# Optimization experiments

Measured on AMD Instinct MI355X. Metric: run time of the kernel, lower is better.

Reference implementation:

```python
import jax, jax.numpy as jnp
import numpy as np

B, M, K = 8192, 1024, 2048
R_LR = 0.1
LMDA = 1e-12
TOL = 0.01          # relative-change convergence threshold from the torch code
MAX_ITERS = 10000   # safety cap (torch loop is uncapped; see notes)


def setup_inputs() -> dict:
    key = jax.random.key(0)
    k_img, k_w = jax.random.split(key)
    img_batch = jax.random.normal(k_img, (B, M), dtype=jnp.float32)
    # U.weight is [M, K]; normalize_weights() normalizes columns (dim=0)
    W = jax.random.normal(k_w, (M, K), dtype=jnp.float32)
    W = W / jnp.linalg.norm(W, axis=0, keepdims=True)
    return {"img_batch": img_batch, "W": W}


def _soft_threshold(x, lmda):
    # F.relu(x - l) - F.relu(-x - l): shrink magnitudes toward zero by l
    return jax.nn.relu(x - lmda) - jax.nn.relu(-x - lmda)


def _inference(img_batch, W):
    Bn, Mn = img_batch.shape
    Kn = W.shape[1]
    # MSELoss(reduction='mean'): dL/dpred = 2*(pred - img)/(B*M)
    scale = 2.0 / (Bn * Mn)

    def cond_fun(state):
        _, it, done = state
        # torch: `while not converged`; nan (first iter, ||old_r||=0) -> not done
        return jnp.logical_and(jnp.logical_not(done), it < MAX_ITERS)

    def body_fun(state):
        r, it, _ = state  # r plays the role of old_r for this step
        pred = r @ W.T                       # [B, M], U(r)
        grad_r = scale * ((pred - img_batch) @ W)  # [B, K], analytic MSE grad
        r_new = _soft_threshold(r - R_LR * grad_r, LMDA)
        ratio = jnp.linalg.norm(r_new - r) / jnp.linalg.norm(r)
        return (r_new, it + 1, ratio < TOL)

    r0 = jnp.zeros((Bn, Kn), dtype=img_batch.dtype)
    r, _, _ = jax.lax.while_loop(
        cond_fun, body_fun, (r0, jnp.array(0, jnp.int32), jnp.array(False)))
    return r


def reference(img_batch, W):
    r = _inference(img_batch, W)   # ISTA loop (no grad flows out, as in torch)
    pred = r @ W.T                 # final decode U(r)
    return (r, pred)
```

## Files before the change

### kernel.cpp

```cpp
#include <hip/hip_runtime.h>

#define NB 8192
#define NM 1024
#define NK 2048

typedef unsigned short ushort_t;
using bf16x8 = __attribute__((ext_vector_type(8))) short;
using f32x4  = __attribute__((ext_vector_type(4))) float;

__device__ __forceinline__ float alpha_const() {
  const double s = 0.1 * (2.0 / 8388608.0);
  return (float)(101.0 * s);
}

__device__ __forceinline__ ushort_t f2bf(float f) {
  union { float f; unsigned u; } v; v.f = f;
  unsigned r = (v.u + 0x7FFFu + ((v.u >> 16) & 1u)) >> 16;
  return (ushort_t)r;
}

__device__ __forceinline__ void gload_lds16(const void* g, void* l) {
  __builtin_amdgcn_global_load_lds(
      (const __attribute__((address_space(1))) unsigned int*)g,
      (__attribute__((address_space(3))) unsigned int*)l, 16, 0, 0);
}

__global__ __launch_bounds__(256)
void prep_w_k(const float* __restrict__ W, ushort_t* __restrict__ Wbf,
              ushort_t* __restrict__ Wt)
{
  __shared__ ushort_t tile[64][65];
  const int tid = threadIdx.x;
  const int bW = blockIdx.x;
  const int m0 = (bW >> 5) * 64, k0 = (bW & 31) * 64;
  const int r = tid >> 2, q = tid & 3;
  ushort_t loc[16];
#pragma unroll
  for (int j = 0; j < 4; ++j) {
    const float4 v = *(const float4*)&W[(size_t)(m0 + r) * NK + k0 + q * 16 + j * 4];
    loc[j * 4 + 0] = f2bf(v.x); loc[j * 4 + 1] = f2bf(v.y);
    loc[j * 4 + 2] = f2bf(v.z); loc[j * 4 + 3] = f2bf(v.w);
  }
#pragma unroll
  for (int j = 0; j < 4; ++j) {
    ushort4 o;
    o.x = loc[j * 4 + 0]; o.y = loc[j * 4 + 1];
    o.z = loc[j * 4 + 2]; o.w = loc[j * 4 + 3];
    *(ushort4*)&Wbf[(size_t)(m0 + r) * NK + k0 + q * 16 + j * 4] = o;
  }
#pragma unroll
  for (int jj = 0; jj < 16; ++jj) tile[r][q * 16 + jj] = loc[jj];
  __syncthreads();
  const int kk = tid >> 2, qq = tid & 3;
#pragma unroll
  for (int j = 0; j < 4; ++j) {
    ushort4 o;
    o.x = tile[qq * 16 + j * 4 + 0][kk];
    o.y = tile[qq * 16 + j * 4 + 1][kk];
    o.z = tile[qq * 16 + j * 4 + 2][kk];
    o.w = tile[qq * 16 + j * 4 + 3][kk];
    *(ushort4*)&Wt[(size_t)(k0 + kk) * NM + m0 + qq * 16 + j * 4] = o;
  }
}

__global__ __launch_bounds__(256)
void qimg_k(const ushort_t* __restrict__ Wbf, ushort_t* __restrict__ Qbf,
            const float* __restrict__ img, ushort_t* __restrict__ imgbf)
{
  __shared__ __align__(128) ushort_t As[64 * 64];
  __shared__ __align__(128) ushort_t Bs[64 * 64];
  const int tid = threadIdx.x;
  const int b = blockIdx.x;

  if (b >= 256) {
    const int base = (b - 256) * 2048;
#pragma unroll
    for (int i = 0; i < 8; ++i) {
      const int idx = base + i * 256 + tid;
      const float4 v = ((const float4*)img)[idx];
      ushort4 o;
      o.x = f2bf(v.x); o.y = f2bf(v.y); o.z = f2bf(v.z); o.w = f2bf(v.w);
      ((ushort4*)imgbf)[idx] = o;
    }
    return;
  }

  const int w = tid >> 6, l = tid & 63;
  const int wm2 = w >> 1, wn2 = w & 1;
  const int bi = b >> 4, bj = b & 15;
  const int i0 = bi * 64, j0 = bj * 64;
  const int l15 = l & 15, l16 = l >> 4;
  const int lr = l >> 3;
  const int lc = (l & 7) * 8;

  f32x4 acc[2][2];
#pragma unroll
  for (int m = 0; m < 2; ++m)
#pragma unroll
    for (int n = 0; n < 2; ++n)
      acc[m][n] = (f32x4){0.f, 0.f, 0.f, 0.f};

  for (int k0 = 0; k0 < NK; k0 += 64) {
#pragma unroll
    for (int c = 0; c < 2; ++c) {
      const int rr = c * 32 + w * 8 + lr;
      const int base = c * 2048 + w * 512;
      gload_lds16(Wbf + (size_t)(i0 + rr) * NK + k0 + lc, &As[base]);
      gload_lds16(Wbf + (size_t)(j0 + rr) * NK + k0 + lc, &Bs[base]);
    }
    __syncthreads();
#pragma unroll
    for (int ks = 0; ks < 2; ++ks) {
      bf16x8 af[2], bfr[2];
#pragma unroll
      for (int m = 0; m < 2; ++m)
        af[m] = *(const bf16x8*)&As[(wm2 * 32 + m * 16 + l15) * 64 + ks * 32 + l16 * 8];
#pragma unroll
      for (int n = 0; n < 2; ++n)
        bfr[n] = *(const bf16x8*)&Bs[(wn2 * 32 + n * 16 + l15) * 64 + ks * 32 + l16 * 8];
#pragma unroll
      for (int m = 0; m < 2; ++m)
#pragma unroll
        for (int n = 0; n < 2; ++n)
          acc[m][n] = __builtin_amdgcn_mfma_f32_16x16x32_bf16(af[m], bfr[n], acc[m][n], 0, 0, 0);
    }
    __syncthreads();
  }

#pragma unroll
  for (int m = 0; m < 2; ++m)
#pragma unroll
    for (int n = 0; n < 2; ++n) {
      const int gr0 = i0 + wm2 * 32 + m * 16 + l16 * 4;
      const int gc  = j0 + wn2 * 32 + n * 16 + l15;
#pragma unroll
      for (int q = 0; q < 4; ++q)
        Qbf[(size_t)(gr0 + q) * NM + gc] = f2bf(acc[m][n][q]);
    }
}

template<int BN>
__device__ __forceinline__
void gemm8ph_body(char* smem,
                  const ushort_t* __restrict__ Aop, const ushort_t* __restrict__ Bop,
                  int KK, int njb, int outld, float* __restrict__ outf,
                  int bid, int nblk)
{
  constexpr int WN  = BN / 4;
  constexpr int NFR = BN / 64;

  const int tid = threadIdx.x;
  const int w = tid >> 6, l = tid & 63;
  const int wm = w >> 2, wn = w & 3;
  const int wg = (bid & 7) * (nblk >> 3) + (bid >> 3);
  const int bi = wg / njb, bj = wg % njb;
  const int i0 = bi * 256, j0 = bj * BN;
  const int l15 = l & 15, l16 = l >> 4;
  const int srow8 = l >> 3;
  const int scb   = (l & 7) << 4;

  const float al = alpha_const();

  ushort_t* ldsA = (ushort_t*)smem;
  ushort_t* ldsB = (ushort_t*)(smem + 65536);
  constexpr int ASTR = 256 * 64;
  constexpr int BSTR = BN * 64;

  f32x4 acc[8][NFR];
#pragma unroll
  for (int m = 0; m < 8; ++m)
#pragma unroll
    for (int n = 0; n < NFR; ++n)
      acc[m][n] = (f32x4){0.f, 0.f, 0.f, 0.f};
  bf16x8 Bf[NFR][2];

  auto SH2 = [&](ushort_t* lb, const ushort_t* g0) {
#pragma unroll
    for (int c = 0; c < 2; ++c) {
      const int row = (w * 2 + c) * 8 + srow8;
      const int sc = (scb ^ ((row & 7) << 4)) >> 1;
      gload_lds16(g0 + (size_t)row * (size_t)KK + sc, lb + (w * 2 + c) * 512);
    }
  };
  auto SH1 = [&](ushort_t* lb, const ushort_t* g0) {
    const int row = w * 8 + srow8;
    const int sc = (scb ^ ((row & 7) << 4)) >> 1;
    gload_lds16(g0 + (size_t)row * (size_t)KK + sc, lb + w * 512);
  };
  auto stA = [&](int buf, int half, int kt) {
    SH2(ldsA + buf * ASTR + half * (128 * 64),
        Aop + (size_t)(i0 + half * 128) * (size_t)KK + (size_t)kt * 64);
  };
  auto stB = [&](int buf, int half, int kt) {
    if constexpr (BN == 256)
      SH2(ldsB + buf * BSTR + half * (128 * 64),
          Bop + (size_t)(j0 + half * 128) * (size_t)KK + (size_t)kt * 64);
    else
      SH1(ldsB + buf * BSTR + half * (64 * 64),
          Bop + (size_t)(j0 + half * 64) * (size_t)KK + (size_t)kt * 64);
  };
  auto rdA = [&](int buf, int R, int ks) -> bf16x8 {
    const int bc = ((ks * 64 + l16 * 16) ^ ((R & 7) << 4)) >> 1;
    return *(const bf16x8*)&ldsA[buf * ASTR + R * 64 + bc];
  };
  auto rdB = [&](int buf, int R, int ks) -> bf16x8 {
    const int bc = ((ks * 64 + l16 * 16) ^ ((R & 7) << 4)) >> 1;
    return *(const bf16x8*)&ldsB[buf * BSTR + R * 64 + bc];
  };

#define VMC_STEADY() do { \
    if constexpr (BN == 256) asm volatile("s_waitcnt vmcnt(4)" ::: "memory"); \
    else                     asm volatile("s_waitcnt vmcnt(2)" ::: "memory"); } while (0)

#define STOREQ(qd)                                                          \
  do {                                                                      \
    _Pragma("unroll")                                                       \
    for (int mm = 0; mm < 2; ++mm) {                                        \
      const int m = (qd) * 2 + mm;                                          \
      const int gr0 = i0 + wm * 128 + m * 16 + l16 * 4;                     \
      _Pragma("unroll")                                                     \
      for (int n = 0; n < NFR; ++n) {                                       \
        const int gc = j0 + wn * WN + n * 16 + l15;                         \
        _Pragma("unroll")                                                   \
        for (int qq = 0; qq < 4; ++qq) {                                    \
          const size_t idx = (size_t)(gr0 + qq) * (size_t)outld + gc;       \
          outf[idx] = al * acc[m][n][qq];                                   \
        }                                                                   \
      }                                                                     \
    }                                                                       \
  } while (0)

#define PHASE(bufc, q, LB, STG, VM, EPI)                                    \
  do {                                                                      \
    if (LB) {                                                               \
      _Pragma("unroll")                                                     \
      for (int n = 0; n < NFR; ++n) {                                       \
        Bf[n][0] = rdB(bufc, wn * WN + n * 16 + l15, 0);                    \
        Bf[n][1] = rdB(bufc, wn * WN + n * 16 + l15, 1);                    \
      }                                                                     \
    }                                                                       \
    bf16x8 a00 = rdA(bufc, wm * 128 + ((q) * 2 + 0) * 16 + l15, 0);         \
    bf16x8 a01 = rdA(bufc, wm * 128 + ((q) * 2 + 0) * 16 + l15, 1);         \
    bf16x8 a10 = rdA(bufc, wm * 128 + ((q) * 2 + 1) * 16 + l15, 0);         \
    bf16x8 a11 = rdA(bufc, wm * 128 + ((q) * 2 + 1) * 16 + l15, 1);         \
    STG;                                                                    \
    if (LB && BN == 256) asm volatile("s_waitcnt lgkmcnt(8)" ::: "memory"); \
    __builtin_amdgcn_s_barrier();                                           \
    asm volatile("s_waitcnt lgkmcnt(0)" ::: "memory");                      \
    __builtin_amdgcn_sched_barrier(0);                                      \
    __builtin_amdgcn_s_setprio(1);                                          \
    _Pragma("unroll")                                                       \
    for (int n = 0; n < NFR; ++n) {                                         \
      acc[(q) * 2 + 0][n] = __builtin_amdgcn_mfma_f32_16x16x32_bf16(        \
          a00, Bf[n][0], acc[(q) * 2 + 0][n], 0, 0, 0);                     \
      acc[(q) * 2 + 0][n] = __builtin_amdgcn_mfma_f32_16x16x32_bf16(        \
          a01, Bf[n][1], acc[(q) * 2 + 0][n], 0, 0, 0);                     \
      acc[(q) * 2 + 1][n] = __builtin_amdgcn_mfma_f32_16x16x32_bf16(        \
          a10, Bf[n][0], acc[(q) * 2 + 1][n], 0, 0, 0);                     \
      acc[(q) * 2 + 1][n] = __builtin_amdgcn_mfma_f32_16x16x32_bf16(        \
          a11, Bf[n][1], acc[(q) * 2 + 1][n], 0, 0, 0);                     \
    }                                                                       \
    __builtin_amdgcn_s_setprio(0);                                          \
    EPI;                                                                    \
    {                                                                       \
      const int _vm = (VM);                                                 \
      if (_vm == 1) VMC_STEADY();                                           \
      else if (_vm == 2) asm volatile("s_waitcnt vmcnt(0)" ::: "memory");   \
    }                                                                       \
    __builtin_amdgcn_s_barrier();                                           \
    __builtin_amdgcn_sched_barrier(0);                                      \
  } while (0)

  const int nt = KK >> 6;
  const int nit = nt >> 1;

  stA(0, 0, 0); stA(0, 1, 0); stB(0, 0, 0); stB(0, 1, 0);
  stB(1, 0, 1); stB(1, 1, 1);
  VMC_STEADY();
  __builtin_amdgcn_s_barrier();
  __builtin_amdgcn_sched_barrier(0);

#pragma unroll 1
  for (int it = 0; it < nit - 1; ++it) {
    const int t1 = 2 * it + 1, t2 = 2 * it + 2, t3 = 2 * it + 3;
    PHASE(0, 0, true,  { stA(1, 0, t1); }, 0, );
    PHASE(0, 1, false, { stA(1, 1, t1); }, 0, );
    PHASE(0, 2, false, { stB(0, 0, t2); }, 0, );
    PHASE(0, 3, false, { stB(0, 1, t2); }, 1, );
    PHASE(1, 0, true,  { stA(0, 0, t2); }, 0, );
    PHASE(1, 1, false, { stA(0, 1, t2); }, 0, );
    PHASE(1, 2, false, { stB(1, 0, t3); }, 0, );
    PHASE(1, 3, false, { stB(1, 1, t3); }, 1, );
  }
  {
    const int t1 = nt - 1;
    PHASE(0, 0, true,  { stA(1, 0, t1); }, 0, );
    PHASE(0, 1, false, { stA(1, 1, t1); }, 0, );
    PHASE(0, 2, false, { }, 0, );
    PHASE(0, 3, false, { }, 2, );
    PHASE(1, 0, true,  { }, 0, STOREQ(0));
    PHASE(1, 1, false, { }, 0, STOREQ(1));
    PHASE(1, 2, false, { }, 0, STOREQ(2));
    PHASE(1, 3, false, { }, 0, STOREQ(3));
  }
#undef PHASE
#undef STOREQ
#undef VMC_STEADY
}

__global__ __launch_bounds__(512, 2)
void finals_k(const ushort_t* __restrict__ imgbf, const ushort_t* __restrict__ Wt,
              const ushort_t* __restrict__ Qbf,
              float* __restrict__ Rr, float* __restrict__ Pp)
{
  __shared__ __align__(1024) char smem[131072];
  const int b = blockIdx.x;
  if (b < 256)
    gemm8ph_body<256>(smem, imgbf, Wt, NM, 8, NK, Rr, b, 256);
  else
    gemm8ph_body<128>(smem, imgbf, Qbf, NM, 8, NM, Pp, b - 256, 256);
}

extern "C" void kernel_launch(void* const* d_in, const int* in_sizes, int n_in,
                              void* d_out, int out_size, void* d_ws, size_t ws_size,
                              hipStream_t stream) {
  (void)in_sizes; (void)n_in; (void)out_size; (void)ws_size;
  const float* img = (const float*)d_in[0];
  const float* W   = (const float*)d_in[1];

  float* Rr = (float*)d_out;
  float* Pp = Rr + (size_t)NB * NK;

  char* ws = (char*)d_ws;
  ushort_t* imgbf = (ushort_t*)(ws + 0);
  ushort_t* Wt    = (ushort_t*)(ws + 16777216);
  ushort_t* Wbf   = (ushort_t*)(ws + 20971520);
  ushort_t* Qbf   = (ushort_t*)(ws + 25165824);

  prep_w_k<<<512, 256, 0, stream>>>(W, Wbf, Wt);

  qimg_k<<<1280, 256, 0, stream>>>(Wbf, Qbf, img, imgbf);

  finals_k<<<512, 512, 0, stream>>>(imgbf, Wt, Qbf, Rr, Pp);
}
```

Before: 92.57 us.

## Fuse W prep and Q GEMM kernels with inter-block ready flags

Merges the W conversion/transpose kernel and the Q GEMM plus image-conversion kernel into one 1280-block launch. Producer blocks publish a per-tile flag with a release store, and GEMM blocks spin on the flags they need before reading Wbf. This removes one kernel launch and the boundary between the two stages, and lets image conversion overlap with waiting. In exchange it relies on producer blocks being scheduled before consumers. The flags are never reset, so on repeat calls consumers may skip the wait and read stale Wbf.

```diff
diff --git a/kernel.cpp b/kernel.cpp
--- a/kernel.cpp
+++ b/kernel.cpp
@@ -3,6 +3,7 @@
 #define NB 8192
 #define NM 1024
 #define NK 2048
+#define MAGIC 0x5AFE0001
 
 typedef unsigned short ushort_t;
 using bf16x8 = __attribute__((ext_vector_type(8))) short;
@@ -26,54 +27,52 @@
 }
 
 __global__ __launch_bounds__(256)
-void prep_w_k(const float* __restrict__ W, ushort_t* __restrict__ Wbf,
-              ushort_t* __restrict__ Wt)
+void prepq_k(const float* __restrict__ W, const float* __restrict__ img,
+             ushort_t* __restrict__ Wbf, ushort_t* __restrict__ Wt,
+             ushort_t* __restrict__ Qbf, ushort_t* __restrict__ imgbf,
+             int* __restrict__ ready)
 {
-  __shared__ ushort_t tile[64][65];
-  const int tid = threadIdx.x;
-  const int bW = blockIdx.x;
-  const int m0 = (bW >> 5) * 64, k0 = (bW & 31) * 64;
-  const int r = tid >> 2, q = tid & 3;
-  ushort_t loc[16];
-#pragma unroll
-  for (int j = 0; j < 4; ++j) {
-    const float4 v = *(const float4*)&W[(size_t)(m0 + r) * NK + k0 + q * 16 + j * 4];
-    loc[j * 4 + 0] = f2bf(v.x); loc[j * 4 + 1] = f2bf(v.y);
-    loc[j * 4 + 2] = f2bf(v.z); loc[j * 4 + 3] = f2bf(v.w);
-  }
-#pragma unroll
-  for (int j = 0; j < 4; ++j) {
-    ushort4 o;
-    o.x = loc[j * 4 + 0]; o.y = loc[j * 4 + 1];
-    o.z = loc[j * 4 + 2]; o.w = loc[j * 4 + 3];
-    *(ushort4*)&Wbf[(size_t)(m0 + r) * NK + k0 + q * 16 + j * 4] = o;
-  }
-#pragma unroll
-  for (int jj = 0; jj < 16; ++jj) tile[r][q * 16 + jj] = loc[jj];
-  __syncthreads();
-  const int kk = tid >> 2, qq = tid & 3;
-#pragma unroll
-  for (int j = 0; j < 4; ++j) {
-    ushort4 o;
-    o.x = tile[qq * 16 + j * 4 + 0][kk];
-    o.y = tile[qq * 16 + j * 4 + 1][kk];
-    o.z = tile[qq * 16 + j * 4 + 2][kk];
-    o.w = tile[qq * 16 + j * 4 + 3][kk];
-    *(ushort4*)&Wt[(size_t)(k0 + kk) * NM + m0 + qq * 16 + j * 4] = o;
-  }
-}
-
-__global__ __launch_bounds__(256)
-void qimg_k(const ushort_t* __restrict__ Wbf, ushort_t* __restrict__ Qbf,
-            const float* __restrict__ img, ushort_t* __restrict__ imgbf)
-{
-  __shared__ __align__(128) ushort_t As[64 * 64];
-  __shared__ __align__(128) ushort_t Bs[64 * 64];
+  __shared__ __align__(128) char smem[16384];
   const int tid = threadIdx.x;
   const int b = blockIdx.x;
 
-  if (b >= 256) {
-    const int base = (b - 256) * 2048;
+  if (b < 512) {
+    ushort_t (*tile)[65] = (ushort_t(*)[65])smem;
+    const int m0 = (b >> 5) * 64, k0 = (b & 31) * 64;
+    const int r = tid >> 2, q = tid & 3;
+    ushort_t loc[16];
+#pragma unroll
+    for (int j = 0; j < 4; ++j) {
+      const float4 v = *(const float4*)&W[(size_t)(m0 + r) * NK + k0 + q * 16 + j * 4];
+      loc[j * 4 + 0] = f2bf(v.x); loc[j * 4 + 1] = f2bf(v.y);
+      loc[j * 4 + 2] = f2bf(v.z); loc[j * 4 + 3] = f2bf(v.w);
+    }
+#pragma unroll
+    for (int j = 0; j < 4; ++j) {
+      ushort4 o;
+      o.x = loc[j * 4 + 0]; o.y = loc[j * 4 + 1];
+      o.z = loc[j * 4 + 2]; o.w = loc[j * 4 + 3];
+      *(ushort4*)&Wbf[(size_t)(m0 + r) * NK + k0 + q * 16 + j * 4] = o;
+    }
+#pragma unroll
+    for (int jj = 0; jj < 16; ++jj) tile[r][q * 16 + jj] = loc[jj];
+    __syncthreads();
+    const int kk = tid >> 2, qq = tid & 3;
+#pragma unroll
+    for (int j = 0; j < 4; ++j) {
+      ushort4 o;
+      o.x = tile[qq * 16 + j * 4 + 0][kk];
+      o.y = tile[qq * 16 + j * 4 + 1][kk];
+      o.z = tile[qq * 16 + j * 4 + 2][kk];
+      o.w = tile[qq * 16 + j * 4 + 3][kk];
+      *(ushort4*)&Wt[(size_t)(k0 + kk) * NM + m0 + qq * 16 + j * 4] = o;
+    }
+    __threadfence();
+    __syncthreads();
+    if (tid == 0)
+      __hip_atomic_store(&ready[b], MAGIC, __ATOMIC_RELEASE,
+                         __HIP_MEMORY_SCOPE_AGENT);
+    const int base = b * 2048;
 #pragma unroll
     for (int i = 0; i < 8; ++i) {
       const int idx = base + i * 256 + tid;
@@ -85,9 +84,38 @@
     return;
   }
 
+  if (b >= 768) {
+    const int base = (b - 256) * 2048;
+#pragma unroll
+    for (int i = 0; i < 8; ++i) {
+      const int idx = base + i * 256 + tid;
+      const float4 v = ((const float4*)img)[idx];
+      ushort4 o;
+      o.x = f2bf(v.x); o.y = f2bf(v.y); o.z = f2bf(v.z); o.w = f2bf(v.w);
+      ((ushort4*)imgbf)[idx] = o;
+    }
+    return;
+  }
+
+  {
+    bool ok;
+    do {
+      const int v0 = __hip_atomic_load(&ready[tid * 2], __ATOMIC_RELAXED,
+                                       __HIP_MEMORY_SCOPE_AGENT);
+      const int v1 = __hip_atomic_load(&ready[tid * 2 + 1], __ATOMIC_RELAXED,
+                                       __HIP_MEMORY_SCOPE_AGENT);
+      ok = (v0 == MAGIC) && (v1 == MAGIC);
+      if (!ok) __builtin_amdgcn_s_sleep(2);
+    } while (!__syncthreads_and(ok));
+    __threadfence();
+  }
+
+  ushort_t* As = (ushort_t*)smem;
+  ushort_t* Bs = (ushort_t*)(smem + 8192);
+  const int bq = b - 512;
   const int w = tid >> 6, l = tid & 63;
   const int wm2 = w >> 1, wn2 = w & 1;
-  const int bi = b >> 4, bj = b & 15;
+  const int bi = bq >> 4, bj = bq & 15;
   const int i0 = bi * 64, j0 = bj * 64;
   const int l15 = l & 15, l16 = l >> 4;
   const int lr = l >> 3;
@@ -336,10 +364,9 @@
   ushort_t* Wt    = (ushort_t*)(ws + 16777216);
   ushort_t* Wbf   = (ushort_t*)(ws + 20971520);
   ushort_t* Qbf   = (ushort_t*)(ws + 25165824);
-
-  prep_w_k<<<512, 256, 0, stream>>>(W, Wbf, Wt);
-
-  qimg_k<<<1280, 256, 0, stream>>>(Wbf, Qbf, img, imgbf);
+  int*      ready = (int*)(ws + 27262976);
+
+  prepq_k<<<1280, 256, 0, stream>>>(W, img, Wbf, Wt, Qbf, imgbf, ready);
 
   finals_k<<<512, 512, 0, stream>>>(imgbf, Wt, Qbf, Rr, Pp);
 }
```

Result: slower. 187.8 us (+102.9%).
